# Optimization experiments

Measured on AMD Instinct MI355X. Metric: run time of the kernel, lower is better.

The kernel has to match this reference:

```python
import jax, jax.numpy as jnp
import numpy as np

B, T, L = 64, 128, 32          # batch, read timesteps, item_len (write phase)
D, R = 256, 1024               # output_dim (= input dim per step), controller rnn_size
N, M = 512, 128                # memory_rows, memory_columns
RH, WH = 1, 1                  # read / write heads
EPS = 1e-8
SCALE = 0.02


def setup_inputs() -> dict:
    key = jax.random.key(0)
    ks = jax.random.split(key, 6)
    in_dim = D + RH * M                      # controller sees [x_t, prev reads]
    head_dim = RH * (M + 6) + WH * (3 * M + 6)  # k,beta,g,s(3),gamma (+erase,add for write)
    return {
        "inputs": jax.random.normal(ks[0], (B, T, D), jnp.float32),
        "W_lstm": jax.random.normal(ks[1], (in_dim, 4 * R), jnp.float32) * SCALE,
        "U_lstm": jax.random.normal(ks[2], (R, 4 * R), jnp.float32) * SCALE,
        "b_lstm": jnp.zeros((4 * R,), jnp.float32),
        "W_heads": jax.random.normal(ks[3], (R, head_dim), jnp.float32) * SCALE,
        "b_heads": jnp.zeros((head_dim,), jnp.float32),
        "W_out": jax.random.normal(ks[4], (R + RH * M, D), jnp.float32) * SCALE,
        "b_out": jnp.zeros((D,), jnp.float32),
    }


def _address(Mem, Mem_norm, k, beta, g, s, gamma, w_prev):
    """NTM content + location addressing. Mem:[B,N,M], returns w:[B,N]."""
    k = jnp.tanh(k)                                   # [B,M]
    beta = jax.nn.softplus(beta)                      # [B,1]
    g = jax.nn.sigmoid(g)                             # [B,1]
    s = jax.nn.softmax(s, axis=-1)                    # [B,3] shifts (-1,0,1)
    gamma = 1.0 + jax.nn.softplus(gamma)              # [B,1]
    # cosine similarity content addressing
    sim = jnp.einsum('bnm,bm->bn', Mem, k) / (
        Mem_norm * jnp.linalg.norm(k, axis=-1, keepdims=True) + EPS)
    w_c = jax.nn.softmax(beta * sim, axis=-1)
    # interpolate with previous weighting
    w_g = g * w_c + (1.0 - g) * w_prev
    # circular convolutional shift over {-1,0,1}
    w_s = (s[:, 0:1] * jnp.roll(w_g, -1, axis=-1)
           + s[:, 1:2] * w_g
           + s[:, 2:3] * jnp.roll(w_g, 1, axis=-1))
    # sharpen
    w_pow = (w_s + EPS) ** gamma
    return w_pow / jnp.sum(w_pow, axis=-1, keepdims=True)


def _run(inputs, W_lstm, U_lstm, b_lstm, W_heads, b_heads, W_out, b_out):
    def step(carry, x_t):
        h, c, reads, w_r, w_w, Mem = carry
        # LSTM controller
        z = jnp.concatenate([x_t, reads], -1) @ W_lstm + h @ U_lstm + b_lstm
        zi, zf, zg, zo = jnp.split(z, 4, axis=-1)
        c = jax.nn.sigmoid(zf) * c + jax.nn.sigmoid(zi) * jnp.tanh(zg)
        h = jax.nn.sigmoid(zo) * jnp.tanh(c)
        # head parameters
        p = h @ W_heads + b_heads
        Mem_norm = jnp.linalg.norm(Mem, axis=-1)  # [B,N]
        new_w_r, new_reads = [], []
        for hh in range(RH):
            o = hh * (M + 6)
            w = _address(Mem, Mem_norm, p[:, o:o + M], p[:, o + M:o + M + 1],
                         p[:, o + M + 1:o + M + 2], p[:, o + M + 2:o + M + 5],
                         p[:, o + M + 5:o + M + 6], w_r[:, hh])
            new_w_r.append(w)
            new_reads.append(jnp.einsum('bn,bnm->bm', w, Mem))
        base, wsz = RH * (M + 6), 3 * M + 6
        new_w_w = []
        for hh in range(WH):
            o = base + hh * wsz
            w = _address(Mem, Mem_norm, p[:, o:o + M], p[:, o + M:o + M + 1],
                         p[:, o + M + 1:o + M + 2], p[:, o + M + 2:o + M + 5],
                         p[:, o + M + 5:o + M + 6], w_w[:, hh])
            erase = jax.nn.sigmoid(p[:, o + M + 6:o + 2 * M + 6])
            add = jnp.tanh(p[:, o + 2 * M + 6:o + 3 * M + 6])
            Mem = Mem * (1.0 - w[:, :, None] * erase[:, None, :]) + w[:, :, None] * add[:, None, :]
            new_w_w.append(w)
        reads = jnp.concatenate(new_reads, -1)
        out = jnp.concatenate([h, reads], -1) @ W_out + b_out
        carry = (h, c, reads, jnp.stack(new_w_r, 1), jnp.stack(new_w_w, 1), Mem)
        return carry, out

    init = (jnp.zeros((B, R)), jnp.zeros((B, R)), jnp.zeros((B, RH * M)),
            jnp.full((B, RH, N), 1.0 / N), jnp.full((B, WH, N), 1.0 / N),
            jnp.full((B, N, M), 1e-6))
    # read phase (inputs) followed by write phase (zero response sheet)
    xs = jnp.concatenate([inputs, jnp.zeros((B, L, D), inputs.dtype)], axis=1)
    xs = jnp.moveaxis(xs, 0, 1)  # [T+L, B, D]
    _, outs = jax.lax.scan(step, init, xs)
    write_outputs = jax.nn.sigmoid(jnp.moveaxis(outs[T:], 0, 1))  # [B, L, D]
    return write_outputs


def reference(inputs, W_lstm, U_lstm, b_lstm, W_heads, b_heads, W_out, b_out):
    return _run(inputs, W_lstm, U_lstm, b_lstm, W_heads, b_heads, W_out, b_out)
```

## Files before the change

### kernel.cpp

```cpp
#include <hip/hip_runtime.h>
#include <hip/hip_fp16.h>
#include <math.h>

#define B 64
#define T_READ 128
#define L_WRITE 32
#define TT 160
#define D 256
#define R 1024
#define N 512
#define M 128
#define HD 524
#define K5K 1152
#define EPS 1e-8f
#define BNM ((size_t)B*N*M)

__device__ __forceinline__ float sigmoidf(float x){ return 1.0f/(1.0f+expf(-x)); }
__device__ __forceinline__ float softplusf(float x){ return (x > 20.f) ? x : log1pf(expf(x)); }

__global__ __launch_bounds__(256) void kx_transpose(const float* __restrict__ x, float* __restrict__ xT){
    __shared__ float tile[64][65];
    const int t = blockIdx.x >> 2, k0 = (blockIdx.x & 3)*64;
    #pragma unroll
    for (int rep = 0; rep < 16; ++rep){
        int idx = rep*256 + threadIdx.x;
        int bl = idx >> 6, kl = idx & 63;
        tile[bl][kl] = x[((size_t)bl*T_READ + t)*D + k0 + kl];
    }
    __syncthreads();
    #pragma unroll
    for (int rep = 0; rep < 16; ++rep){
        int idx = rep*256 + threadIdx.x;
        int kl = idx >> 6, bl = idx & 63;
        xT[((size_t)t*D + k0 + kl)*64 + bl] = tile[bl][kl];
    }
}

__global__ __launch_bounds__(256) void kpack_w(const float* __restrict__ Wl, const float* __restrict__ Ul,
                                               __half* __restrict__ Wreh){
    const int k = blockIdx.x;
    const float* src = (k < 384) ? (Wl + (size_t)k*4096) : (Ul + (size_t)(k-384)*4096);
    #pragma unroll
    for (int it = 0; it < 16; ++it){
        int j = it*256 + threadIdx.x;
        int bk = j >> 4, r = j & 15, q = r >> 2, i = r & 3;
        Wreh[((size_t)bk*1408 + k)*16 + r] = __float2half_rn(src[q*1024 + bk*4 + i]);
    }
}

__global__ __launch_bounds__(256) void kpack_wh(const float* __restrict__ Wh, __half* __restrict__ Whh){
    const int k = blockIdx.x;
    for (int j = threadIdx.x; j < HD; j += 256)
        Whh[(size_t)k*HD + j] = __float2half_rn(Wh[(size_t)k*HD + j]);
}

__global__ void k_init(float* ht, float* c_t, float* rp, float* wst, __half* Mem){
    size_t idx = (size_t)blockIdx.x*blockDim.x + threadIdx.x;
    size_t stride = (size_t)gridDim.x*blockDim.x;
    const __half mi = __float2half(1e-6f);
    for (size_t i = idx; i < BNM; i += stride) Mem[i] = mi;
    for (size_t i = idx; i < R*64; i += stride){ ht[i]=0.f; c_t[i]=0.f; }
    for (size_t i = idx; i < 4*128*64; i += stride) rp[i] = 0.f;
    for (size_t i = idx; i < 2*B*N; i += stride) wst[i] = 1.f/512.f;
}

__global__ __launch_bounds__(1024) void k1_z(
    const float* __restrict__ xT, const __half* __restrict__ Wreh, const float* __restrict__ bl,
    float* __restrict__ ht, float* __restrict__ c_t, const float* __restrict__ rp,
    float* __restrict__ hist, int t)
{
    __shared__ float smem[8192 + 16384];
    const int bk = blockIdx.x;
    const int tid = threadIdx.x, lane = tid & 63, w = tid >> 6;

    for (int e = tid; e < 8192; e += 1024){
        float s = rp[e] + rp[8192+e] + rp[16384+e] + rp[24576+e];
        smem[e] = s;
        if (t > T_READ && (e >> 10) == bk)
            hist[((size_t)(t-1-T_READ)*K5K + 1024 + (e>>6))*64 + (e&63)] = s;
    }
    __syncthreads();

    const int r0 = bk*4;
    const int rd = (t < T_READ);
    const int kn = rd ? 88 : 72;
    const int k0 = rd ? w*88 : 256 + w*72;
    const __half* wbase = Wreh + ((size_t)bk*1408 + k0)*16;
    float acc[16];
    #pragma unroll
    for (int i = 0; i < 16; ++i) acc[i] = 0.f;
    #pragma unroll 4
    for (int kk = 0; kk < kn; ++kk){
        int k = k0 + kk;
        float a;
        if (k < 256)      a = xT[((size_t)t*256 + k)*64 + lane];
        else if (k < 384) a = smem[(k-256)*64 + lane];
        else              a = ht[(size_t)(k-384)*64 + lane];
        float4 raw0 = *reinterpret_cast<const float4*>(wbase + (size_t)kk*16);
        float4 raw1 = *reinterpret_cast<const float4*>(wbase + (size_t)kk*16 + 8);
        const __half2* h0 = reinterpret_cast<const __half2*>(&raw0);
        const __half2* h1 = reinterpret_cast<const __half2*>(&raw1);
        float2 f;
        f = __half22float2(h0[0]); acc[0] += a*f.x; acc[1] += a*f.y;
        f = __half22float2(h0[1]); acc[2] += a*f.x; acc[3] += a*f.y;
        f = __half22float2(h0[2]); acc[4] += a*f.x; acc[5] += a*f.y;
        f = __half22float2(h0[3]); acc[6] += a*f.x; acc[7] += a*f.y;
        f = __half22float2(h1[0]); acc[8] += a*f.x; acc[9] += a*f.y;
        f = __half22float2(h1[1]); acc[10]+= a*f.x; acc[11]+= a*f.y;
        f = __half22float2(h1[2]); acc[12]+= a*f.x; acc[13]+= a*f.y;
        f = __half22float2(h1[3]); acc[14]+= a*f.x; acc[15]+= a*f.y;
    }
    float* comb = smem + 8192;
    #pragma unroll
    for (int j = 0; j < 16; ++j) comb[(w*16 + j)*64 + lane] = acc[j];
    __syncthreads();
    if (tid < 256){
        int i = tid >> 6, b2 = tid & 63;
        float g4[4];
        #pragma unroll
        for (int q = 0; q < 4; ++q){
            float s = bl[q*1024 + r0 + i];
            #pragma unroll
            for (int ks = 0; ks < 16; ++ks) s += comb[(ks*16 + q*4 + i)*64 + b2];
            g4[q] = s;
        }
        int ri = (r0 + i)*64 + b2;
        float cn = sigmoidf(g4[1])*c_t[ri] + sigmoidf(g4[0])*tanhf(g4[2]);
        float hn = sigmoidf(g4[3])*tanhf(cn);
        c_t[ri] = cn;
        ht[ri] = hn;
        if (t >= T_READ) hist[((size_t)(t-T_READ)*K5K + r0 + i)*64 + b2] = hn;
    }
}

__global__ __launch_bounds__(256) void k2_heads(
    const float* __restrict__ ht, const __half* __restrict__ Whh, float* __restrict__ pp)
{
    const int lane = threadIdx.x & 63;
    const int wid  = blockIdx.x*4 + (threadIdx.x >> 6);
    const int cg = wid % 131, ks = wid / 131;
    const int j0 = cg*4;
    const int k0 = ks*64;
    float ax=0.f, ay=0.f, az=0.f, aw=0.f;
    #pragma unroll 4
    for (int k = k0; k < k0+64; ++k){
        float a = ht[(size_t)k*64 + lane];
        float2 raw = *reinterpret_cast<const float2*>(Whh + (size_t)k*HD + j0);
        const __half2* hp = reinterpret_cast<const __half2*>(&raw);
        float2 w01 = __half22float2(hp[0]), w23 = __half22float2(hp[1]);
        ax += a*w01.x; ay += a*w01.y; az += a*w23.x; aw += a*w23.y;
    }
    float* dst = pp + ((size_t)lane*16 + ks)*HD + j0;
    dst[0]=ax; dst[1]=ay; dst[2]=az; dst[3]=aw;
}

__global__ __launch_bounds__(512) void k2b_final(
    const float* __restrict__ pp, const float* __restrict__ bh,
    float* __restrict__ khat, float* __restrict__ scal, float* __restrict__ eal)
{
    const int b = blockIdx.x;
    const int col = threadIdx.x;
    if (col < HD){
        const float* pp_b = pp + (size_t)b*16*HD;
        float v = bh[col];
        #pragma unroll
        for (int ks = 0; ks < 16; ++ks) v += pp_b[ks*HD + col];
        if (col < 128)       khat[b*256 + col] = tanhf(v);
        else if (col < 134){ int i = col-128; scal[b*16 + i]     = (i==0)?softplusf(v):(i==1)?sigmoidf(v):(i==5)?1.f+softplusf(v):v; }
        else if (col < 262)  khat[b*256 + 128 + (col-134)] = tanhf(v);
        else if (col < 268){ int i = col-262; scal[b*16 + 8 + i] = (i==0)?softplusf(v):(i==1)?sigmoidf(v):(i==5)?1.f+softplusf(v):v; }
        else if (col < 396)  eal[b*256 + (col-268)]        = sigmoidf(v);
        else                 eal[b*256 + 128 + (col-396)]  = tanhf(v);
    }
}

__global__ __launch_bounds__(512) void k3_dots(
    const float* __restrict__ khat, const __half* __restrict__ Mem,
    float* __restrict__ mnorm, float* __restrict__ dots)
{
    __shared__ float kh[256];
    const int b = blockIdx.x >> 3, nq = blockIdx.x & 7;
    const int tid = threadIdx.x, lane = tid & 63, w = tid >> 6;
    if (tid < 256) kh[tid] = khat[b*256 + tid];
    __syncthreads();
    float2 kr  = reinterpret_cast<const float2*>(kh)[lane];
    float2 kw2 = reinterpret_cast<const float2*>(kh + 128)[lane];
    #pragma unroll 2
    for (int i = 0; i < 8; ++i){
        int n = nq*64 + w*8 + i;
        const __half* mrow = Mem + ((size_t)b*N + n)*M;
        __half2 mh = *reinterpret_cast<const __half2*>(mrow + lane*2);
        float2 mv = __half22float2(mh);
        float s2 = mv.x*mv.x + mv.y*mv.y;
        float dr = mv.x*kr.x + mv.y*kr.y;
        float dw = mv.x*kw2.x + mv.y*kw2.y;
        #pragma unroll
        for (int off = 32; off; off >>= 1){
            s2 += __shfl_xor(s2, off);
            dr += __shfl_xor(dr, off);
            dw += __shfl_xor(dw, off);
        }
        if (lane == 0){
            mnorm[b*N + n] = sqrtf(s2);
            dots[(b*2+0)*N + n] = dr;
            dots[(b*2+1)*N + n] = dw;
        }
    }
}

__device__ __forceinline__ float blk_sum8g(float v, volatile float* red8, int lane, int wgi){
    #pragma unroll
    for (int off = 32; off; off >>= 1) v += __shfl_xor(v, off);
    if (lane == 0) red8[wgi] = v;
    __syncthreads();
    float r = red8[0]+red8[1]+red8[2]+red8[3]+red8[4]+red8[5]+red8[6]+red8[7];
    __syncthreads();
    return r;
}
__device__ __forceinline__ float blk_max8g(float v, volatile float* red8, int lane, int wgi){
    #pragma unroll
    for (int off = 32; off; off >>= 1) v = fmaxf(v, __shfl_xor(v, off));
    if (lane == 0) red8[wgi] = v;
    __syncthreads();
    float r = fmaxf(fmaxf(fmaxf(red8[0],red8[1]),fmaxf(red8[2],red8[3])),
                    fmaxf(fmaxf(red8[4],red8[5]),fmaxf(red8[6],red8[7])));
    __syncthreads();
    return r;
}

__global__ __launch_bounds__(1024) void k4_addr(
    const float* __restrict__ khat, const float* __restrict__ scal, const float* __restrict__ ealg,
    const float* __restrict__ mnorm, const float* __restrict__ dots,
    float* __restrict__ wst, __half* __restrict__ Mem, float* __restrict__ rp, int t)
{
    __shared__ float kh[256];
    __shared__ float sc[16];
    __shared__ float eal[256];
    __shared__ float wfin[1024];
    __shared__ float wgbuf[1024];
    __shared__ float red8[2][8];
    __shared__ float racc_s[1024];
    const int b = blockIdx.x >> 2, nq = blockIdx.x & 3;
    const int tid = threadIdx.x, lane = tid & 63;

    if (tid < 256)      kh[tid]        = khat[b*256 + tid];
    else if (tid < 272) sc[tid-256]    = scal[b*16 + (tid-256)];
    else if (tid < 528) eal[tid-272]   = ealg[b*256 + (tid-272)];
    __syncthreads();

    {
        const int g = tid >> 9;
        const int n = tid & 511;
        const int wgi = (tid >> 6) & 7;
        float* wgl = wgbuf + g*512;
        volatile float* r8 = red8[g];

        float kv = (n < 128) ? kh[g*128 + n] : 0.f;
        float knm = sqrtf(blk_sum8g(kv*kv, r8, lane, wgi));
        float beta = sc[g*8+0], gg = sc[g*8+1], gamma = sc[g*8+5];
        float s0r = sc[g*8+2], s1r = sc[g*8+3], s2r = sc[g*8+4];
        float smx = fmaxf(s0r, fmaxf(s1r, s2r));
        float e0 = expf(s0r-smx), e1 = expf(s1r-smx), e2 = expf(s2r-smx);
        float esum = e0+e1+e2;
        float s0 = e0/esum, s1 = e1/esum, s2 = e2/esum;

        float sim = dots[(b*2+g)*N + n] / (mnorm[b*N + n]*knm + EPS);
        float aa = beta * sim;
        float amax = blk_max8g(aa, r8, lane, wgi);
        float ev = expf(aa - amax);
        float wc = ev / blk_sum8g(ev, r8, lane, wgi);

        const float* wpr = wst + ((size_t)((t&1)*2 + g))*(B*N);
        float*       wnx = wst + ((size_t)(((t+1)&1)*2 + g))*(B*N);
        float wprev = wpr[b*N + n];
        float wgv = gg*wc + (1.f - gg)*wprev;
        wgl[n] = wgv; __syncthreads();
        float wsv = s0*wgl[(n+1)&511] + s1*wgv + s2*wgl[(n-1)&511];
        float wp2 = powf(wsv + EPS, gamma);
        float wsum = blk_sum8g(wp2, r8, lane, wgi);
        float wv = wp2 / wsum;
        wfin[g*512 + n] = wv;
        if (nq == 0) wnx[b*N + n] = wv;
        __syncthreads();
    }

    {
        const int m = tid & 127, ns = tid >> 7;
        const float e  = eal[m];
        const float ad = eal[128 + m];
        float racc = 0.f;
        #pragma unroll 4
        for (int i2 = 0; i2 < 16; ++i2){
            int nn = nq*128 + i2*8 + ns;
            size_t idx = ((size_t)b*N + nn)*M + m;
            float v = __half2float(Mem[idx]);
            float wr = wfin[nn], ww = wfin[512 + nn];
            racc += wr*v;
            Mem[idx] = __float2half_rn(v*(1.f - ww*e) + ww*ad);
        }
        racc_s[tid] = racc;
        __syncthreads();
        if (tid < 128){
            float s = 0.f;
            #pragma unroll
            for (int g2 = 0; g2 < 8; ++g2) s += racc_s[g2*128 + tid];
            rp[(size_t)nq*8192 + tid*64 + b] = s;
        }
    }
}

__global__ __launch_bounds__(256) void k_fin(const float* __restrict__ rp, float* __restrict__ hist){
    int e = blockIdx.x*256 + threadIdx.x;
    float s = rp[e] + rp[8192+e] + rp[16384+e] + rp[24576+e];
    hist[((size_t)31*K5K + 1024 + (e>>6))*64 + (e&63)] = s;
}

__global__ __launch_bounds__(512) void k5_out(
    const float* __restrict__ hist, const float* __restrict__ Wo, const float* __restrict__ bo,
    float* __restrict__ out)
{
    __shared__ float smem[16384];
    const int tid = threadIdx.x, lane = tid & 63, w = tid >> 6;
    const int l = blockIdx.x >> 3, jg = blockIdx.x & 7;
    const int j0 = jg*32;
    float acc[32];
    #pragma unroll
    for (int i = 0; i < 32; ++i) acc[i] = 0.f;
    const int k0 = w*144;
    #pragma unroll 2
    for (int kk = 0; kk < 144; ++kk){
        int k = k0 + kk;
        float a = hist[((size_t)l*K5K + k)*64 + lane];
        const float* wrow = Wo + (size_t)k*D + j0;
        #pragma unroll
        for (int qq = 0; qq < 8; ++qq){
            float4 wv = *reinterpret_cast<const float4*>(wrow + qq*4);
            acc[qq*4+0] += a*wv.x; acc[qq*4+1] += a*wv.y;
            acc[qq*4+2] += a*wv.z; acc[qq*4+3] += a*wv.w;
        }
    }
    __syncthreads();
    #pragma unroll
    for (int c = 0; c < 32; ++c) smem[(w*32 + c)*64 + lane] = acc[c];
    __syncthreads();
    {
        const int b2 = tid >> 3, jq = tid & 7;
        float4 ov;
        float* po = (float*)&ov;
        #pragma unroll
        for (int i = 0; i < 4; ++i){
            int c = jq*4 + i;
            float s = bo[j0 + c];
            #pragma unroll
            for (int ks = 0; ks < 8; ++ks) s += smem[(ks*32 + c)*64 + b2];
            po[i] = sigmoidf(s);
        }
        *reinterpret_cast<float4*>(out + ((size_t)b2*L_WRITE + l)*D + j0 + jq*4) = ov;
    }
}

extern "C" void kernel_launch(void* const* d_in, const int* in_sizes, int n_in,
                              void* d_out, int out_size, void* d_ws, size_t ws_size,
                              hipStream_t stream)
{
    const float* x   = (const float*)d_in[0];
    const float* Wl  = (const float*)d_in[1];
    const float* Ul  = (const float*)d_in[2];
    const float* bl  = (const float*)d_in[3];
    const float* Wh  = (const float*)d_in[4];
    const float* bh  = (const float*)d_in[5];
    const float* Wo  = (const float*)d_in[6];
    const float* bo  = (const float*)d_in[7];
    float* out = (float*)d_out;

    float* ws = (float*)d_ws;
    float* xT    = ws; ws += (size_t)T_READ*D*64;
    __half* Wreh = (__half*)ws; ws += (size_t)1408*4096/2;
    __half* Whh  = (__half*)ws; ws += (size_t)1024*HD/2 + 64;
    float* ht    = ws; ws += (size_t)R*64;
    float* c_t   = ws; ws += (size_t)R*64;
    float* pp    = ws; ws += (size_t)B*16*HD;
    float* khat  = ws; ws += (size_t)B*256;
    float* scal  = ws; ws += (size_t)B*16;
    float* eal   = ws; ws += (size_t)B*256;
    float* mnorm = ws; ws += (size_t)B*N;
    float* dots  = ws; ws += (size_t)B*2*N;
    float* wst   = ws; ws += (size_t)4*B*N;
    __half* Mem  = (__half*)ws; ws += BNM/2;
    float* rp    = ws; ws += (size_t)4*128*64;
    float* hist  = ws; ws += (size_t)L_WRITE*K5K*64;

    hipLaunchKernelGGL(kx_transpose, dim3(T_READ*4), dim3(256), 0, stream, x, xT);
    hipLaunchKernelGGL(kpack_w,      dim3(1408),     dim3(256), 0, stream, Wl, Ul, Wreh);
    hipLaunchKernelGGL(kpack_wh,     dim3(1024),     dim3(256), 0, stream, Wh, Whh);
    hipLaunchKernelGGL(k_init,       dim3(2048),     dim3(256), 0, stream, ht, c_t, rp, wst, Mem);

    for (int t = 0; t < TT; ++t){
        hipLaunchKernelGGL(k1_z,      dim3(256), dim3(1024), 0, stream, xT, Wreh, bl, ht, c_t, rp, hist, t);
        hipLaunchKernelGGL(k2_heads,  dim3(524), dim3(256),  0, stream, ht, Whh, pp);
        hipLaunchKernelGGL(k2b_final, dim3(64),  dim3(512),  0, stream, pp, bh, khat, scal, eal);
        hipLaunchKernelGGL(k3_dots,   dim3(512), dim3(512),  0, stream, khat, Mem, mnorm, dots);
        hipLaunchKernelGGL(k4_addr,   dim3(256), dim3(1024), 0, stream, khat, scal, eal, mnorm, dots, wst, Mem, rp, t);
    }
    hipLaunchKernelGGL(k_fin,  dim3(32),  dim3(256), 0, stream, rp, hist);
    hipLaunchKernelGGL(k5_out, dim3(256), dim3(512), 0, stream, hist, Wo, bo, out);
}
```

Before: 11.56 ms.

## Fuse per-step head and memory kernels, cutting launches from five to three per step

Each timestep now runs three kernels instead of five. The head projection and its nonlinear finalisation are merged into one kernel that reduces across K in shared memory, and the dot/norm pass is folded into the addressing and memory-update kernel. That kernel now uses one block per batch element rather than four, so it no longer needs the 4-way partial read buffer and the separate final reduction kernel, and the weight state updates in place without double buffering. The aim is to remove launch overhead and global round-trips. The cost is that the memory kernel drops to 64 blocks, which leaves many CUs idle during the Mem read/update sweep.

```diff
diff --git a/kernel.cpp b/kernel.cpp
--- a/kernel.cpp
+++ b/kernel.cpp
@@ -54,32 +54,24 @@
         Whh[(size_t)k*HD + j] = __float2half_rn(Wh[(size_t)k*HD + j]);
 }
 
-__global__ void k_init(float* ht, float* c_t, float* rp, float* wst, __half* Mem){
+__global__ void k_init(float* ht, float* c_t, float* readsbuf, float* wst, __half* Mem){
     size_t idx = (size_t)blockIdx.x*blockDim.x + threadIdx.x;
     size_t stride = (size_t)gridDim.x*blockDim.x;
     const __half mi = __float2half(1e-6f);
     for (size_t i = idx; i < BNM; i += stride) Mem[i] = mi;
     for (size_t i = idx; i < R*64; i += stride){ ht[i]=0.f; c_t[i]=0.f; }
-    for (size_t i = idx; i < 4*128*64; i += stride) rp[i] = 0.f;
+    for (size_t i = idx; i < M*64; i += stride) readsbuf[i] = 0.f;
     for (size_t i = idx; i < 2*B*N; i += stride) wst[i] = 1.f/512.f;
 }
 
 __global__ __launch_bounds__(1024) void k1_z(
     const float* __restrict__ xT, const __half* __restrict__ Wreh, const float* __restrict__ bl,
-    float* __restrict__ ht, float* __restrict__ c_t, const float* __restrict__ rp,
+    float* __restrict__ ht, float* __restrict__ c_t, const float* __restrict__ readsbuf,
     float* __restrict__ hist, int t)
 {
-    __shared__ float smem[8192 + 16384];
+    __shared__ float comb[16384];
     const int bk = blockIdx.x;
     const int tid = threadIdx.x, lane = tid & 63, w = tid >> 6;
-
-    for (int e = tid; e < 8192; e += 1024){
-        float s = rp[e] + rp[8192+e] + rp[16384+e] + rp[24576+e];
-        smem[e] = s;
-        if (t > T_READ && (e >> 10) == bk)
-            hist[((size_t)(t-1-T_READ)*K5K + 1024 + (e>>6))*64 + (e&63)] = s;
-    }
-    __syncthreads();
 
     const int r0 = bk*4;
     const int rd = (t < T_READ);
@@ -94,7 +86,7 @@
         int k = k0 + kk;
         float a;
         if (k < 256)      a = xT[((size_t)t*256 + k)*64 + lane];
-        else if (k < 384) a = smem[(k-256)*64 + lane];
+        else if (k < 384) a = readsbuf[(k-256)*64 + lane];
         else              a = ht[(size_t)(k-384)*64 + lane];
         float4 raw0 = *reinterpret_cast<const float4*>(wbase + (size_t)kk*16);
         float4 raw1 = *reinterpret_cast<const float4*>(wbase + (size_t)kk*16 + 8);
@@ -110,7 +102,6 @@
         f = __half22float2(h1[2]); acc[12]+= a*f.x; acc[13]+= a*f.y;
         f = __half22float2(h1[3]); acc[14]+= a*f.x; acc[15]+= a*f.y;
     }
-    float* comb = smem + 8192;
     #pragma unroll
     for (int j = 0; j < 16; ++j) comb[(w*16 + j)*64 + lane] = acc[j];
     __syncthreads();
@@ -133,38 +124,31 @@
     }
 }
 
-__global__ __launch_bounds__(256) void k2_heads(
-    const float* __restrict__ ht, const __half* __restrict__ Whh, float* __restrict__ pp)
-{
-    const int lane = threadIdx.x & 63;
-    const int wid  = blockIdx.x*4 + (threadIdx.x >> 6);
-    const int cg = wid % 131, ks = wid / 131;
-    const int j0 = cg*4;
-    const int k0 = ks*64;
-    float ax=0.f, ay=0.f, az=0.f, aw=0.f;
+__global__ __launch_bounds__(512) void k2f(
+    const float* __restrict__ ht, const __half* __restrict__ Whh, const float* __restrict__ bh,
+    float* __restrict__ khat, float* __restrict__ scal, float* __restrict__ eal)
+{
+    __shared__ float part[8][2][64];
+    const int tid = threadIdx.x, lane = tid & 63, w = tid >> 6;
+    const int col0 = blockIdx.x*2;
+    const int k0 = w*128;
+    float a0 = 0.f, a1 = 0.f;
     #pragma unroll 4
-    for (int k = k0; k < k0+64; ++k){
+    for (int k = k0; k < k0+128; ++k){
         float a = ht[(size_t)k*64 + lane];
-        float2 raw = *reinterpret_cast<const float2*>(Whh + (size_t)k*HD + j0);
-        const __half2* hp = reinterpret_cast<const __half2*>(&raw);
-        float2 w01 = __half22float2(hp[0]), w23 = __half22float2(hp[1]);
-        ax += a*w01.x; ay += a*w01.y; az += a*w23.x; aw += a*w23.y;
-    }
-    float* dst = pp + ((size_t)lane*16 + ks)*HD + j0;
-    dst[0]=ax; dst[1]=ay; dst[2]=az; dst[3]=aw;
-}
-
-__global__ __launch_bounds__(512) void k2b_final(
-    const float* __restrict__ pp, const float* __restrict__ bh,
-    float* __restrict__ khat, float* __restrict__ scal, float* __restrict__ eal)
-{
-    const int b = blockIdx.x;
-    const int col = threadIdx.x;
-    if (col < HD){
-        const float* pp_b = pp + (size_t)b*16*HD;
+        __half2 wv = *reinterpret_cast<const __half2*>(Whh + (size_t)k*HD + col0);
+        float2 f = __half22float2(wv);
+        a0 += a*f.x; a1 += a*f.y;
+    }
+    part[w][0][lane] = a0;
+    part[w][1][lane] = a1;
+    __syncthreads();
+    if (tid < 128){
+        int c = tid >> 6, b = tid & 63;
+        int col = col0 + c;
         float v = bh[col];
         #pragma unroll
-        for (int ks = 0; ks < 16; ++ks) v += pp_b[ks*HD + col];
+        for (int w2 = 0; w2 < 8; ++w2) v += part[w2][c][b];
         if (col < 128)       khat[b*256 + col] = tanhf(v);
         else if (col < 134){ int i = col-128; scal[b*16 + i]     = (i==0)?softplusf(v):(i==1)?sigmoidf(v):(i==5)?1.f+softplusf(v):v; }
         else if (col < 262)  khat[b*256 + 128 + (col-134)] = tanhf(v);
@@ -174,40 +158,6 @@
     }
 }
 
-__global__ __launch_bounds__(512) void k3_dots(
-    const float* __restrict__ khat, const __half* __restrict__ Mem,
-    float* __restrict__ mnorm, float* __restrict__ dots)
-{
-    __shared__ float kh[256];
-    const int b = blockIdx.x >> 3, nq = blockIdx.x & 7;
-    const int tid = threadIdx.x, lane = tid & 63, w = tid >> 6;
-    if (tid < 256) kh[tid] = khat[b*256 + tid];
-    __syncthreads();
-    float2 kr  = reinterpret_cast<const float2*>(kh)[lane];
-    float2 kw2 = reinterpret_cast<const float2*>(kh + 128)[lane];
-    #pragma unroll 2
-    for (int i = 0; i < 8; ++i){
-        int n = nq*64 + w*8 + i;
-        const __half* mrow = Mem + ((size_t)b*N + n)*M;
-        __half2 mh = *reinterpret_cast<const __half2*>(mrow + lane*2);
-        float2 mv = __half22float2(mh);
-        float s2 = mv.x*mv.x + mv.y*mv.y;
-        float dr = mv.x*kr.x + mv.y*kr.y;
-        float dw = mv.x*kw2.x + mv.y*kw2.y;
-        #pragma unroll
-        for (int off = 32; off; off >>= 1){
-            s2 += __shfl_xor(s2, off);
-            dr += __shfl_xor(dr, off);
-            dw += __shfl_xor(dw, off);
-        }
-        if (lane == 0){
-            mnorm[b*N + n] = sqrtf(s2);
-            dots[(b*2+0)*N + n] = dr;
-            dots[(b*2+1)*N + n] = dw;
-        }
-    }
-}
-
 __device__ __forceinline__ float blk_sum8g(float v, volatile float* red8, int lane, int wgi){
     #pragma unroll
     for (int off = 32; off; off >>= 1) v += __shfl_xor(v, off);
@@ -228,24 +178,53 @@
     return r;
 }
 
-__global__ __launch_bounds__(1024) void k4_addr(
+__global__ __launch_bounds__(1024) void kmem(
     const float* __restrict__ khat, const float* __restrict__ scal, const float* __restrict__ ealg,
-    const float* __restrict__ mnorm, const float* __restrict__ dots,
-    float* __restrict__ wst, __half* __restrict__ Mem, float* __restrict__ rp, int t)
+    float* __restrict__ wst, __half* __restrict__ Mem,
+    float* __restrict__ readsbuf, float* __restrict__ hist, int t)
 {
     __shared__ float kh[256];
     __shared__ float sc[16];
     __shared__ float eal[256];
+    __shared__ float mnorm_s[512];
+    __shared__ float dots_s[2][512];
     __shared__ float wfin[1024];
     __shared__ float wgbuf[1024];
     __shared__ float red8[2][8];
     __shared__ float racc_s[1024];
-    const int b = blockIdx.x >> 2, nq = blockIdx.x & 3;
+    const int b = blockIdx.x;
     const int tid = threadIdx.x, lane = tid & 63;
 
-    if (tid < 256)      kh[tid]        = khat[b*256 + tid];
-    else if (tid < 272) sc[tid-256]    = scal[b*16 + (tid-256)];
-    else if (tid < 528) eal[tid-272]   = ealg[b*256 + (tid-272)];
+    if (tid < 256)      kh[tid]      = khat[b*256 + tid];
+    else if (tid < 272) sc[tid-256]  = scal[b*16 + (tid-256)];
+    else if (tid < 528) eal[tid-272] = ealg[b*256 + (tid-272)];
+    __syncthreads();
+
+    {
+        const int w16 = tid >> 6;
+        float2 kr  = reinterpret_cast<const float2*>(kh)[lane];
+        float2 kw2 = reinterpret_cast<const float2*>(kh + 128)[lane];
+        #pragma unroll 2
+        for (int i = 0; i < 32; ++i){
+            int n = w16*32 + i;
+            __half2 mh = *reinterpret_cast<const __half2*>(Mem + ((size_t)b*N + n)*M + lane*2);
+            float2 mv = __half22float2(mh);
+            float s2 = mv.x*mv.x + mv.y*mv.y;
+            float dr = mv.x*kr.x + mv.y*kr.y;
+            float dw = mv.x*kw2.x + mv.y*kw2.y;
+            #pragma unroll
+            for (int off = 32; off; off >>= 1){
+                s2 += __shfl_xor(s2, off);
+                dr += __shfl_xor(dr, off);
+                dw += __shfl_xor(dw, off);
+            }
+            if (lane == 0){
+                mnorm_s[n] = sqrtf(s2);
+                dots_s[0][n] = dr;
+                dots_s[1][n] = dw;
+            }
+        }
+    }
     __syncthreads();
 
     {
@@ -264,15 +243,14 @@
         float esum = e0+e1+e2;
         float s0 = e0/esum, s1 = e1/esum, s2 = e2/esum;
 
-        float sim = dots[(b*2+g)*N + n] / (mnorm[b*N + n]*knm + EPS);
+        float sim = dots_s[g][n] / (mnorm_s[n]*knm + EPS);
         float aa = beta * sim;
         float amax = blk_max8g(aa, r8, lane, wgi);
         float ev = expf(aa - amax);
         float wc = ev / blk_sum8g(ev, r8, lane, wgi);
 
-        const float* wpr = wst + ((size_t)((t&1)*2 + g))*(B*N);
-        float*       wnx = wst + ((size_t)(((t+1)&1)*2 + g))*(B*N);
-        float wprev = wpr[b*N + n];
+        float* wbuf = wst + (size_t)g*(B*N);
+        float wprev = wbuf[b*N + n];
         float wgv = gg*wc + (1.f - gg)*wprev;
         wgl[n] = wgv; __syncthreads();
         float wsv = s0*wgl[(n+1)&511] + s1*wgv + s2*wgl[(n-1)&511];
@@ -280,7 +258,7 @@
         float wsum = blk_sum8g(wp2, r8, lane, wgi);
         float wv = wp2 / wsum;
         wfin[g*512 + n] = wv;
-        if (nq == 0) wnx[b*N + n] = wv;
+        wbuf[b*N + n] = wv;
         __syncthreads();
     }
 
@@ -290,11 +268,11 @@
         const float ad = eal[128 + m];
         float racc = 0.f;
         #pragma unroll 4
-        for (int i2 = 0; i2 < 16; ++i2){
-            int nn = nq*128 + i2*8 + ns;
-            size_t idx = ((size_t)b*N + nn)*M + m;
+        for (int i = 0; i < 64; ++i){
+            int n = i*8 + ns;
+            size_t idx = ((size_t)b*N + n)*M + m;
             float v = __half2float(Mem[idx]);
-            float wr = wfin[nn], ww = wfin[512 + nn];
+            float wr = wfin[n], ww = wfin[512 + n];
             racc += wr*v;
             Mem[idx] = __float2half_rn(v*(1.f - ww*e) + ww*ad);
         }
@@ -304,15 +282,10 @@
             float s = 0.f;
             #pragma unroll
             for (int g2 = 0; g2 < 8; ++g2) s += racc_s[g2*128 + tid];
-            rp[(size_t)nq*8192 + tid*64 + b] = s;
-        }
-    }
-}
-
-__global__ __launch_bounds__(256) void k_fin(const float* __restrict__ rp, float* __restrict__ hist){
-    int e = blockIdx.x*256 + threadIdx.x;
-    float s = rp[e] + rp[8192+e] + rp[16384+e] + rp[24576+e];
-    hist[((size_t)31*K5K + 1024 + (e>>6))*64 + (e&63)] = s;
+            readsbuf[tid*64 + b] = s;
+            if (t >= T_READ) hist[((size_t)(t-T_READ)*K5K + 1024 + tid)*64 + b] = s;
+        }
+    }
 }
 
 __global__ __launch_bounds__(512) void k5_out(
@@ -379,29 +352,23 @@
     __half* Whh  = (__half*)ws; ws += (size_t)1024*HD/2 + 64;
     float* ht    = ws; ws += (size_t)R*64;
     float* c_t   = ws; ws += (size_t)R*64;
-    float* pp    = ws; ws += (size_t)B*16*HD;
     float* khat  = ws; ws += (size_t)B*256;
     float* scal  = ws; ws += (size_t)B*16;
     float* eal   = ws; ws += (size_t)B*256;
-    float* mnorm = ws; ws += (size_t)B*N;
-    float* dots  = ws; ws += (size_t)B*2*N;
-    float* wst   = ws; ws += (size_t)4*B*N;
+    float* readsbuf = ws; ws += (size_t)M*64;
+    float* wst   = ws; ws += (size_t)2*B*N;
     __half* Mem  = (__half*)ws; ws += BNM/2;
-    float* rp    = ws; ws += (size_t)4*128*64;
     float* hist  = ws; ws += (size_t)L_WRITE*K5K*64;
 
     hipLaunchKernelGGL(kx_transpose, dim3(T_READ*4), dim3(256), 0, stream, x, xT);
     hipLaunchKernelGGL(kpack_w,      dim3(1408),     dim3(256), 0, stream, Wl, Ul, Wreh);
     hipLaunchKernelGGL(kpack_wh,     dim3(1024),     dim3(256), 0, stream, Wh, Whh);
-    hipLaunchKernelGGL(k_init,       dim3(2048),     dim3(256), 0, stream, ht, c_t, rp, wst, Mem);
+    hipLaunchKernelGGL(k_init,       dim3(2048),     dim3(256), 0, stream, ht, c_t, readsbuf, wst, Mem);
 
     for (int t = 0; t < TT; ++t){
-        hipLaunchKernelGGL(k1_z,      dim3(256), dim3(1024), 0, stream, xT, Wreh, bl, ht, c_t, rp, hist, t);
-        hipLaunchKernelGGL(k2_heads,  dim3(524), dim3(256),  0, stream, ht, Whh, pp);
-        hipLaunchKernelGGL(k2b_final, dim3(64),  dim3(512),  0, stream, pp, bh, khat, scal, eal);
-        hipLaunchKernelGGL(k3_dots,   dim3(512), dim3(512),  0, stream, khat, Mem, mnorm, dots);
-        hipLaunchKernelGGL(k4_addr,   dim3(256), dim3(1024), 0, stream, khat, scal, eal, mnorm, dots, wst, Mem, rp, t);
-    }
-    hipLaunchKernelGGL(k_fin,  dim3(32),  dim3(256), 0, stream, rp, hist);
+        hipLaunchKernelGGL(k1_z,  dim3(256), dim3(1024), 0, stream, xT, Wreh, bl, ht, c_t, readsbuf, hist, t);
+        hipLaunchKernelGGL(k2f,   dim3(262), dim3(512),  0, stream, ht, Whh, bh, khat, scal, eal);
+        hipLaunchKernelGGL(kmem,  dim3(64),  dim3(1024), 0, stream, khat, scal, eal, wst, Mem, readsbuf, hist, t);
+    }
     hipLaunchKernelGGL(k5_out, dim3(256), dim3(512), 0, stream, hist, Wo, bo, out);
 }
```

Measured after the change: 14.27 ms. 1.23x slower.

## Fuse head projection with its reduction and split memory update over more blocks

Applied to the files above, without the earlier changes.

The head projection and its cross-split reduction kernel are merged into a single kernel. Each block now handles two output columns, reduces its eight partial sums in shared memory and applies the activations itself. This removes one launch per timestep and the global partial-sum buffer. The addressing/memory-update kernel now uses 8 blocks per batch row instead of 4, each covering 64 memory rows, so the read partials grow to 8 slices that are summed downstream. This adds parallelism in the memory pass, but every block redoes the full addressing softmax, so that redundant work doubles.

```diff
diff --git a/kernel.cpp b/kernel.cpp
--- a/kernel.cpp
+++ b/kernel.cpp
@@ -60,8 +60,8 @@
     const __half mi = __float2half(1e-6f);
     for (size_t i = idx; i < BNM; i += stride) Mem[i] = mi;
     for (size_t i = idx; i < R*64; i += stride){ ht[i]=0.f; c_t[i]=0.f; }
-    for (size_t i = idx; i < 4*128*64; i += stride) rp[i] = 0.f;
-    for (size_t i = idx; i < 2*B*N; i += stride) wst[i] = 1.f/512.f;
+    for (size_t i = idx; i < 8*128*64; i += stride) rp[i] = 0.f;
+    for (size_t i = idx; i < 4*B*N; i += stride) wst[i] = 1.f/512.f;
 }
 
 __global__ __launch_bounds__(1024) void k1_z(
@@ -74,7 +74,9 @@
     const int tid = threadIdx.x, lane = tid & 63, w = tid >> 6;
 
     for (int e = tid; e < 8192; e += 1024){
-        float s = rp[e] + rp[8192+e] + rp[16384+e] + rp[24576+e];
+        float s = 0.f;
+        #pragma unroll
+        for (int p = 0; p < 8; ++p) s += rp[p*8192 + e];
         smem[e] = s;
         if (t > T_READ && (e >> 10) == bk)
             hist[((size_t)(t-1-T_READ)*K5K + 1024 + (e>>6))*64 + (e&63)] = s;
@@ -133,38 +135,31 @@
     }
 }
 
-__global__ __launch_bounds__(256) void k2_heads(
-    const float* __restrict__ ht, const __half* __restrict__ Whh, float* __restrict__ pp)
-{
-    const int lane = threadIdx.x & 63;
-    const int wid  = blockIdx.x*4 + (threadIdx.x >> 6);
-    const int cg = wid % 131, ks = wid / 131;
-    const int j0 = cg*4;
-    const int k0 = ks*64;
-    float ax=0.f, ay=0.f, az=0.f, aw=0.f;
+__global__ __launch_bounds__(512) void k2f(
+    const float* __restrict__ ht, const __half* __restrict__ Whh, const float* __restrict__ bh,
+    float* __restrict__ khat, float* __restrict__ scal, float* __restrict__ eal)
+{
+    __shared__ float part[8][2][64];
+    const int tid = threadIdx.x, lane = tid & 63, w = tid >> 6;
+    const int col0 = blockIdx.x*2;
+    const int k0 = w*128;
+    float a0 = 0.f, a1 = 0.f;
     #pragma unroll 4
-    for (int k = k0; k < k0+64; ++k){
+    for (int k = k0; k < k0+128; ++k){
         float a = ht[(size_t)k*64 + lane];
-        float2 raw = *reinterpret_cast<const float2*>(Whh + (size_t)k*HD + j0);
-        const __half2* hp = reinterpret_cast<const __half2*>(&raw);
-        float2 w01 = __half22float2(hp[0]), w23 = __half22float2(hp[1]);
-        ax += a*w01.x; ay += a*w01.y; az += a*w23.x; aw += a*w23.y;
-    }
-    float* dst = pp + ((size_t)lane*16 + ks)*HD + j0;
-    dst[0]=ax; dst[1]=ay; dst[2]=az; dst[3]=aw;
-}
-
-__global__ __launch_bounds__(512) void k2b_final(
-    const float* __restrict__ pp, const float* __restrict__ bh,
-    float* __restrict__ khat, float* __restrict__ scal, float* __restrict__ eal)
-{
-    const int b = blockIdx.x;
-    const int col = threadIdx.x;
-    if (col < HD){
-        const float* pp_b = pp + (size_t)b*16*HD;
+        __half2 wv = *reinterpret_cast<const __half2*>(Whh + (size_t)k*HD + col0);
+        float2 f = __half22float2(wv);
+        a0 += a*f.x; a1 += a*f.y;
+    }
+    part[w][0][lane] = a0;
+    part[w][1][lane] = a1;
+    __syncthreads();
+    if (tid < 128){
+        int c = tid >> 6, b = tid & 63;
+        int col = col0 + c;
         float v = bh[col];
         #pragma unroll
-        for (int ks = 0; ks < 16; ++ks) v += pp_b[ks*HD + col];
+        for (int w2 = 0; w2 < 8; ++w2) v += part[w2][c][b];
         if (col < 128)       khat[b*256 + col] = tanhf(v);
         else if (col < 134){ int i = col-128; scal[b*16 + i]     = (i==0)?softplusf(v):(i==1)?sigmoidf(v):(i==5)?1.f+softplusf(v):v; }
         else if (col < 262)  khat[b*256 + 128 + (col-134)] = tanhf(v);
@@ -240,12 +235,12 @@
     __shared__ float wgbuf[1024];
     __shared__ float red8[2][8];
     __shared__ float racc_s[1024];
-    const int b = blockIdx.x >> 2, nq = blockIdx.x & 3;
+    const int b = blockIdx.x >> 3, nq = blockIdx.x & 7;
     const int tid = threadIdx.x, lane = tid & 63;
 
-    if (tid < 256)      kh[tid]        = khat[b*256 + tid];
-    else if (tid < 272) sc[tid-256]    = scal[b*16 + (tid-256)];
-    else if (tid < 528) eal[tid-272]   = ealg[b*256 + (tid-272)];
+    if (tid < 256)      kh[tid]      = khat[b*256 + tid];
+    else if (tid < 272) sc[tid-256]  = scal[b*16 + (tid-256)];
+    else if (tid < 528) eal[tid-272] = ealg[b*256 + (tid-272)];
     __syncthreads();
 
     {
@@ -290,8 +285,8 @@
         const float ad = eal[128 + m];
         float racc = 0.f;
         #pragma unroll 4
-        for (int i2 = 0; i2 < 16; ++i2){
-            int nn = nq*128 + i2*8 + ns;
+        for (int i2 = 0; i2 < 8; ++i2){
+            int nn = nq*64 + i2*8 + ns;
             size_t idx = ((size_t)b*N + nn)*M + m;
             float v = __half2float(Mem[idx]);
             float wr = wfin[nn], ww = wfin[512 + nn];
@@ -311,7 +306,9 @@
 
 __global__ __launch_bounds__(256) void k_fin(const float* __restrict__ rp, float* __restrict__ hist){
     int e = blockIdx.x*256 + threadIdx.x;
-    float s = rp[e] + rp[8192+e] + rp[16384+e] + rp[24576+e];
+    float s = 0.f;
+    #pragma unroll
+    for (int p = 0; p < 8; ++p) s += rp[p*8192 + e];
     hist[((size_t)31*K5K + 1024 + (e>>6))*64 + (e&63)] = s;
 }
 
@@ -379,7 +376,6 @@
     __half* Whh  = (__half*)ws; ws += (size_t)1024*HD/2 + 64;
     float* ht    = ws; ws += (size_t)R*64;
     float* c_t   = ws; ws += (size_t)R*64;
-    float* pp    = ws; ws += (size_t)B*16*HD;
     float* khat  = ws; ws += (size_t)B*256;
     float* scal  = ws; ws += (size_t)B*16;
     float* eal   = ws; ws += (size_t)B*256;
@@ -387,7 +383,7 @@
     float* dots  = ws; ws += (size_t)B*2*N;
     float* wst   = ws; ws += (size_t)4*B*N;
     __half* Mem  = (__half*)ws; ws += BNM/2;
-    float* rp    = ws; ws += (size_t)4*128*64;
+    float* rp    = ws; ws += (size_t)8*128*64;
     float* hist  = ws; ws += (size_t)L_WRITE*K5K*64;
 
     hipLaunchKernelGGL(kx_transpose, dim3(T_READ*4), dim3(256), 0, stream, x, xT);
@@ -396,11 +392,10 @@
     hipLaunchKernelGGL(k_init,       dim3(2048),     dim3(256), 0, stream, ht, c_t, rp, wst, Mem);
 
     for (int t = 0; t < TT; ++t){
-        hipLaunchKernelGGL(k1_z,      dim3(256), dim3(1024), 0, stream, xT, Wreh, bl, ht, c_t, rp, hist, t);
-        hipLaunchKernelGGL(k2_heads,  dim3(524), dim3(256),  0, stream, ht, Whh, pp);
-        hipLaunchKernelGGL(k2b_final, dim3(64),  dim3(512),  0, stream, pp, bh, khat, scal, eal);
-        hipLaunchKernelGGL(k3_dots,   dim3(512), dim3(512),  0, stream, khat, Mem, mnorm, dots);
-        hipLaunchKernelGGL(k4_addr,   dim3(256), dim3(1024), 0, stream, khat, scal, eal, mnorm, dots, wst, Mem, rp, t);
+        hipLaunchKernelGGL(k1_z,    dim3(256), dim3(1024), 0, stream, xT, Wreh, bl, ht, c_t, rp, hist, t);
+        hipLaunchKernelGGL(k2f,     dim3(262), dim3(512),  0, stream, ht, Whh, bh, khat, scal, eal);
+        hipLaunchKernelGGL(k3_dots, dim3(512), dim3(512),  0, stream, khat, Mem, mnorm, dots);
+        hipLaunchKernelGGL(k4_addr, dim3(512), dim3(1024), 0, stream, khat, scal, eal, mnorm, dots, wst, Mem, rp, t);
     }
     hipLaunchKernelGGL(k_fin,  dim3(32),  dim3(256), 0, stream, rp, hist);
     hipLaunchKernelGGL(k5_out, dim3(256), dim3(512), 0, stream, hist, Wo, bo, out);
```

After: 11.28 ms. 1.02x faster.
